# Kernel tuning notes

Measured on AMD Instinct MI355X. Metric: run time of the kernel, lower is better.

## Reference

```python
import jax, jax.numpy as jnp
import numpy as np


def setup_inputs() -> dict:
    key = jax.random.key(0)
    ks = jax.random.split(key, 7)
    B, C, H, W = 4, 64, 64, 64
    d = C // 8
    s = C ** -0.5  # 1x1-conv fan-in init scale
    x = jax.random.normal(ks[0], (B, C, H, W), jnp.float32)
    Wq = jax.random.normal(ks[1], (d, C), jnp.float32) * s
    bq = jnp.zeros((d,), jnp.float32)
    Wk = jax.random.normal(ks[2], (d, C), jnp.float32) * s
    bk = jnp.zeros((d,), jnp.float32)
    Wv = jax.random.normal(ks[3], (C, C), jnp.float32) * s
    bv = jnp.zeros((C,), jnp.float32)
    return {"x": x, "Wq": Wq, "bq": bq, "Wk": Wk, "bk": bk, "Wv": Wv, "bv": bv}


def reference(x, Wq, bq, Wk, bk, Wv, bv):
    B, C, H, W = x.shape
    N = H * W
    xf = x.reshape(B, C, N)                               # [B,C,N]
    # 1x1 convs == per-pixel channel matmuls
    q = jnp.einsum('dc,bcn->bnd', Wq, xf) + bq            # [B,N,d]
    k = jnp.einsum('dc,bcn->bnd', Wk, xf) + bk            # [B,N,d]
    v = jnp.einsum('ec,bcn->ben', Wv, xf) + bv[:, None]   # [B,C,N]
    # pairwise relative position offsets over flattened spatial grid
    idx = jnp.arange(N)
    col = (idx % W).astype(x.dtype)
    row = (idx // W).astype(x.dtype)
    col_diff = col[None, :] - col[:, None]                # [N,N], col_j - col_i
    row_diff = row[None, :] - row[:, None]                # [N,N]
    # scores = Q . (K + rel_pos folded into first two key channels)
    scores = jnp.einsum('bnd,bmd->bnm', q, k)             # [B,N,N]
    scores = scores + q[:, :, 0, None] * col_diff[None] + q[:, :, 1, None] * row_diff[None]
    attn = jax.nn.softmax(scores, axis=-1)                # softmax over keys
    out = jnp.einsum('bcm,bnm->bcn', v, attn)             # [B,C,N]
    return out.reshape(B, C, H, W)
```

## Files before the change

kernel.cpp:

```cpp
#include <hip/hip_runtime.h>

#define BB 4
#define CC 64
#define NN 4096

typedef __attribute__((ext_vector_type(8))) short short8;
typedef __attribute__((ext_vector_type(4))) float f32x4;
typedef __attribute__((ext_vector_type(4))) unsigned uint4v;

__device__ inline ushort f2bf(float x) {
    unsigned u = __float_as_uint(x);
    return (ushort)((u + 0x7fff + ((u >> 16) & 1)) >> 16);
}
__device__ inline float bf2f(ushort h) { return __uint_as_float(((unsigned)h) << 16); }

__device__ inline unsigned cvt_pk_bf16(float a, float b) {
    unsigned r;
    asm("v_cvt_pk_bf16_f32 %0, %1, %2" : "=v"(r) : "v"(a), "v"(b));
    return r;
}


__global__ __launch_bounds__(256) void qkv_kernel(
    const float* __restrict__ x,
    const float* __restrict__ Wq, const float* __restrict__ bq,
    const float* __restrict__ Wk, const float* __restrict__ bk,
    const float* __restrict__ Wv, const float* __restrict__ bv,
    ushort* __restrict__ qTp, ushort* __restrict__ kTp, ushort* __restrict__ vsw)
{
    const int blk = blockIdx.x;
    const int tid = threadIdx.x;

    if (blk < 64) {
        const int idx = blk * 256 + tid;
        const int b = idx >> 12, n = idx & (NN - 1);
        const float* xb = x + (size_t)b * CC * NN + n;
        float sq[8], sk[8];
#pragma unroll
        for (int d = 0; d < 8; ++d) { sq[d] = bq[d]; sk[d] = bk[d]; }
#pragma unroll 8
        for (int c = 0; c < CC; ++c) {
            const float xc = xb[c * NN];
#pragma unroll
            for (int d = 0; d < 8; ++d) {
                sq[d] += Wq[d * CC + c] * xc;
                sk[d] += Wk[d * CC + c] * xc;
            }
        }
        ushort hq[32], hk[32];
#pragma unroll
        for (int i = 0; i < 32; ++i) { hq[i] = 0; hk[i] = 0; }
#pragma unroll
        for (int d = 0; d < 8; ++d) { hq[d] = f2bf(sq[d]); hk[d] = f2bf(sk[d]); }
        hq[8]  = hq[0];
        hq[9]  = hq[1];
        hq[10] = f2bf(sq[0] - bf2f(hq[0]));
        hq[11] = f2bf(sq[1] - bf2f(hq[1]));
        const float col = (float)(n & 63), row = (float)(n >> 6);
        hk[8] = f2bf(col); hk[9] = f2bf(row); hk[10] = hk[8]; hk[11] = hk[9];

        uint4* dq = (uint4*)(qTp + (size_t)(b * NN + n) * 32);
        uint4* dk = (uint4*)(kTp + (size_t)(b * NN + n) * 32);
        const uint4* s4q = (const uint4*)hq;
        const uint4* s4k = (const uint4*)hk;
#pragma unroll
        for (int i = 0; i < 4; ++i) { dq[i] = s4q[i]; dk[i] = s4k[i]; }
        return;
    }

    const int w2 = blk - 64;
    const int pix = w2 >> 3, ec = w2 & 7;
    const int wvid = tid >> 6, lane = tid & 63;
    const int eu = __builtin_amdgcn_readfirstlane(ec * 4 + wvid);
    const int idx = pix * 64 + lane;
    const int b = idx >> 12, n = idx & (NN - 1);
    const float* xb = x + (size_t)b * CC * NN + n;
    float s0 = bv[eu], s1 = bv[eu + 32];
#pragma unroll 8
    for (int c = 0; c < CC; ++c) {
        const float xc = xb[c * NN];
        s0 += Wv[eu * CC + c] * xc;
        s1 += Wv[(eu + 32) * CC + c] * xc;
    }
    const int j = n & 63, t = n >> 6;
    const int kg = j >> 4, qd = (j >> 2) & 3, r = j & 3;
    const int sb = kg >> 1, jj = ((kg & 1) << 2) | r;
    const size_t tb = (size_t)(b * 64 + t) * 4096;
    const int e2 = eu + 32;
    vsw[tb + (size_t)(((sb * 4 + (eu >> 4)) * 64 + qd * 16 + (eu & 15)) * 8 + jj)] = f2bf(s0);
    vsw[tb + (size_t)(((sb * 4 + (e2 >> 4)) * 64 + qd * 16 + (e2 & 15)) * 8 + jj)] = f2bf(s1);
}

__global__ __launch_bounds__(512, 4) void attn_kernel(
    const ushort* __restrict__ qTp, const ushort* __restrict__ kTp,
    const ushort* __restrict__ vsw, float* __restrict__ out)
{
    const int blk = blockIdx.x;
    const int xcd = blk & 7, i8 = blk >> 3;
    const int b  = xcd >> 1;
    const int nq = (((xcd & 1) << 6) | i8) << 5;
    const int tid = threadIdx.x;
    const int wv = tid >> 6, lane = tid & 63;
    const int nn = lane & 15, quad = lane >> 4;

    __shared__ float Cb[8][1024];
    __shared__ float Mx[8][32];
    __shared__ float Db[8][32];
    __shared__ float dn[32];

    const short8 qf0 = *(const short8*)(qTp + ((size_t)(b * NN + nq + nn) * 32 + quad * 8));
    const short8 qf1 = *(const short8*)(qTp + ((size_t)(b * NN + nq + 16 + nn) * 32 + quad * 8));
    const ushort* kb = kTp + (size_t)b * NN * 32;

    float Ml0 = -1e30f, Ml1 = -1e30f;
    for (int t8 = 0; t8 < 8; ++t8) {
        const int t = wv * 8 + t8;
#pragma unroll
        for (int kg = 0; kg < 4; ++kg) {
            const short8 kf = *(const short8*)(kb + ((size_t)(t * 64 + kg * 16 + nn) * 32 + quad * 8));
            const f32x4 S0 = __builtin_amdgcn_mfma_f32_16x16x32_bf16(kf, qf0, (f32x4){0.f,0.f,0.f,0.f}, 0, 0, 0);
            const f32x4 S1 = __builtin_amdgcn_mfma_f32_16x16x32_bf16(kf, qf1, (f32x4){0.f,0.f,0.f,0.f}, 0, 0, 0);
            Ml0 = fmaxf(Ml0, fmaxf(fmaxf(S0[0], S0[1]), fmaxf(S0[2], S0[3])));
            Ml1 = fmaxf(Ml1, fmaxf(fmaxf(S1[0], S1[1]), fmaxf(S1[2], S1[3])));
        }
    }
    Ml0 = fmaxf(Ml0, __shfl_xor(Ml0, 16, 64));
    Ml0 = fmaxf(Ml0, __shfl_xor(Ml0, 32, 64));
    Ml1 = fmaxf(Ml1, __shfl_xor(Ml1, 16, 64));
    Ml1 = fmaxf(Ml1, __shfl_xor(Ml1, 32, 64));
    if (quad == 0) { Mx[wv][nn] = Ml0; Mx[wv][16 + nn] = Ml1; }
    __syncthreads();
    float M0 = Mx[0][nn], M1 = Mx[0][16 + nn];
#pragma unroll
    for (int w = 1; w < 8; ++w) { M0 = fmaxf(M0, Mx[w][nn]); M1 = fmaxf(M1, Mx[w][16 + nn]); }
    const f32x4 nM0 = {-M0, -M0, -M0, -M0};
    const f32x4 nM1 = {-M1, -M1, -M1, -M1};

    f32x4 acc0[4], acc1[4];
#pragma unroll
    for (int g = 0; g < 4; ++g) {
        acc0[g] = (f32x4){0.f,0.f,0.f,0.f};
        acc1[g] = (f32x4){0.f,0.f,0.f,0.f};
    }
    float dl0 = 0.f, dl1 = 0.f;

    for (int t8 = 0; t8 < 8; ++t8) {
        const int t = wv * 8 + t8;
        unsigned pw0[8], pw1[8];
#pragma unroll
        for (int kg = 0; kg < 4; ++kg) {
            const short8 kf = *(const short8*)(kb + ((size_t)(t * 64 + kg * 16 + nn) * 32 + quad * 8));
            const f32x4 S0 = __builtin_amdgcn_mfma_f32_16x16x32_bf16(kf, qf0, nM0, 0, 0, 0);
            const f32x4 S1 = __builtin_amdgcn_mfma_f32_16x16x32_bf16(kf, qf1, nM1, 0, 0, 0);
            const float w00 = __expf(S0[0]), w01 = __expf(S0[1]);
            const float w02 = __expf(S0[2]), w03 = __expf(S0[3]);
            const float w10 = __expf(S1[0]), w11 = __expf(S1[1]);
            const float w12 = __expf(S1[2]), w13 = __expf(S1[3]);
            dl0 += (w00 + w01) + (w02 + w03);
            dl1 += (w10 + w11) + (w12 + w13);
            pw0[2 * kg]     = cvt_pk_bf16(w00, w01);
            pw0[2 * kg + 1] = cvt_pk_bf16(w02, w03);
            pw1[2 * kg]     = cvt_pk_bf16(w10, w11);
            pw1[2 * kg + 1] = cvt_pk_bf16(w12, w13);
        }
        const uint4v u00 = {pw0[0], pw0[1], pw0[2], pw0[3]};
        const uint4v u01 = {pw0[4], pw0[5], pw0[6], pw0[7]};
        const uint4v u10 = {pw1[0], pw1[1], pw1[2], pw1[3]};
        const uint4v u11 = {pw1[4], pw1[5], pw1[6], pw1[7]};
        const short8 a00 = __builtin_bit_cast(short8, u00);
        const short8 a01 = __builtin_bit_cast(short8, u01);
        const short8 a10 = __builtin_bit_cast(short8, u10);
        const short8 a11 = __builtin_bit_cast(short8, u11);

        const ushort* vb = vsw + (size_t)(b * 64 + t) * 4096;
#pragma unroll
        for (int g = 0; g < 4; ++g) {
            const short8 vf = *(const short8*)(vb + g * 512 + lane * 8);
            acc0[g] = __builtin_amdgcn_mfma_f32_16x16x32_bf16(a00, vf, acc0[g], 0, 0, 0);
            acc1[g] = __builtin_amdgcn_mfma_f32_16x16x32_bf16(a10, vf, acc1[g], 0, 0, 0);
        }
#pragma unroll
        for (int g = 0; g < 4; ++g) {
            const short8 vf = *(const short8*)(vb + 2048 + g * 512 + lane * 8);
            acc0[g] = __builtin_amdgcn_mfma_f32_16x16x32_bf16(a01, vf, acc0[g], 0, 0, 0);
            acc1[g] = __builtin_amdgcn_mfma_f32_16x16x32_bf16(a11, vf, acc1[g], 0, 0, 0);
        }
    }

    dl0 += __shfl_xor(dl0, 16, 64); dl0 += __shfl_xor(dl0, 32, 64);
    dl1 += __shfl_xor(dl1, 16, 64); dl1 += __shfl_xor(dl1, 32, 64);
    if (quad == 0) { Db[wv][nn] = dl0; Db[wv][16 + nn] = dl1; }

#pragma unroll
    for (int g = 0; g < 4; ++g)
#pragma unroll
        for (int r = 0; r < 4; ++r)
            Cb[wv][(g * 4 + r) * 64 + lane] = acc0[g][r];
    __syncthreads();

    if (tid < 32) {
        float s = Db[0][tid];
#pragma unroll
        for (int w = 1; w < 8; ++w) s += Db[w][tid];
        dn[tid] = s;
    }
    __syncthreads();

#pragma unroll
    for (int it = 0; it < 2; ++it) {
        const int e = tid + it * 512;
        const int q = e & 15, c = e >> 4;
        const int src = ((c >> 4) * 4 + (q & 3)) * 64 + (q >> 2) * 16 + (c & 15);
        float v = Cb[0][src];
#pragma unroll
        for (int w = 1; w < 8; ++w) v += Cb[w][src];
        out[(size_t)(b * CC + c) * NN + nq + q] = v / dn[q];
    }
    __syncthreads();

#pragma unroll
    for (int g = 0; g < 4; ++g)
#pragma unroll
        for (int r = 0; r < 4; ++r)
            Cb[wv][(g * 4 + r) * 64 + lane] = acc1[g][r];
    __syncthreads();

#pragma unroll
    for (int it = 0; it < 2; ++it) {
        const int e = tid + it * 512;
        const int q = e & 15, c = e >> 4;
        const int src = ((c >> 4) * 4 + (q & 3)) * 64 + (q >> 2) * 16 + (c & 15);
        float v = Cb[0][src];
#pragma unroll
        for (int w = 1; w < 8; ++w) v += Cb[w][src];
        out[(size_t)(b * CC + c) * NN + nq + 16 + q] = v / dn[16 + q];
    }
}

extern "C" void kernel_launch(void* const* d_in, const int* in_sizes, int n_in,
                              void* d_out, int out_size, void* d_ws, size_t ws_size,
                              hipStream_t stream) {
    const float* x  = (const float*)d_in[0];
    const float* Wq = (const float*)d_in[1];
    const float* bq = (const float*)d_in[2];
    const float* Wk = (const float*)d_in[3];
    const float* bk = (const float*)d_in[4];
    const float* Wv = (const float*)d_in[5];
    const float* bv = (const float*)d_in[6];
    float* out = (float*)d_out;

    ushort* ws  = (ushort*)d_ws;
    ushort* qTp = ws;
    ushort* kTp = ws + (size_t)BB * NN * 32;
    ushort* vsw = ws + (size_t)2 * BB * NN * 32;

    qkv_kernel<<<2112, 256, 0, stream>>>(x, Wq, bq, Wk, bk, Wv, bv, qTp, kTp, vsw);
    attn_kernel<<<512, 512, 0, stream>>>(qTp, kTp, vsw, out);
}
```

Before: 114.3 us.

## Replace two-pass softmax max with online lazy-rescaled softmax; widen V projection per thread

The attention kernel no longer runs a full first pass over all keys to find the row max. It seeds the running max from the first tile and then rescales the accumulators and denominator only when a tile's max exceeds the current one. A final cross-wave merge rescales each wave's partials to the global max. This removes about half of the QK^T MFMA work and K loads, at the cost of per-tile max reductions, shuffles and occasional rescale branches. Separately, the V projection now computes four output channels per thread instead of two, halving the number of V blocks launched.

```diff
diff --git a/kernel.cpp b/kernel.cpp
--- a/kernel.cpp
+++ b/kernel.cpp
@@ -69,26 +69,31 @@
     }
 
     const int w2 = blk - 64;
-    const int pix = w2 >> 3, ec = w2 & 7;
-    const int wvid = tid >> 6, lane = tid & 63;
-    const int eu = __builtin_amdgcn_readfirstlane(ec * 4 + wvid);
+    const int pix = w2 >> 2, ec = w2 & 3;
+    const int lane = tid & 63;
+    const int eu = __builtin_amdgcn_readfirstlane(ec * 4 + (tid >> 6));
     const int idx = pix * 64 + lane;
     const int b = idx >> 12, n = idx & (NN - 1);
     const float* xb = x + (size_t)b * CC * NN + n;
-    float s0 = bv[eu], s1 = bv[eu + 32];
+    float s0 = bv[eu], s1 = bv[eu + 16], s2 = bv[eu + 32], s3 = bv[eu + 48];
 #pragma unroll 8
     for (int c = 0; c < CC; ++c) {
         const float xc = xb[c * NN];
         s0 += Wv[eu * CC + c] * xc;
-        s1 += Wv[(eu + 32) * CC + c] * xc;
+        s1 += Wv[(eu + 16) * CC + c] * xc;
+        s2 += Wv[(eu + 32) * CC + c] * xc;
+        s3 += Wv[(eu + 48) * CC + c] * xc;
     }
     const int j = n & 63, t = n >> 6;
     const int kg = j >> 4, qd = (j >> 2) & 3, r = j & 3;
     const int sb = kg >> 1, jj = ((kg & 1) << 2) | r;
     const size_t tb = (size_t)(b * 64 + t) * 4096;
-    const int e2 = eu + 32;
-    vsw[tb + (size_t)(((sb * 4 + (eu >> 4)) * 64 + qd * 16 + (eu & 15)) * 8 + jj)] = f2bf(s0);
-    vsw[tb + (size_t)(((sb * 4 + (e2 >> 4)) * 64 + qd * 16 + (e2 & 15)) * 8 + jj)] = f2bf(s1);
+    const float sv[4] = {s0, s1, s2, s3};
+#pragma unroll
+    for (int u = 0; u < 4; ++u) {
+        const int e = eu + u * 16;
+        vsw[tb + (size_t)(((sb * 4 + (e >> 4)) * 64 + qd * 16 + (e & 15)) * 8 + jj)] = f2bf(sv[u]);
+    }
 }
 
 __global__ __launch_bounds__(512, 4) void attn_kernel(
@@ -112,29 +117,24 @@
     const short8 qf1 = *(const short8*)(qTp + ((size_t)(b * NN + nq + 16 + nn) * 32 + quad * 8));
     const ushort* kb = kTp + (size_t)b * NN * 32;
 
-    float Ml0 = -1e30f, Ml1 = -1e30f;
-    for (int t8 = 0; t8 < 8; ++t8) {
-        const int t = wv * 8 + t8;
+    float m0 = -1e30f, m1 = -1e30f;
+    {
+        const int t = wv * 8;
 #pragma unroll
         for (int kg = 0; kg < 4; ++kg) {
             const short8 kf = *(const short8*)(kb + ((size_t)(t * 64 + kg * 16 + nn) * 32 + quad * 8));
             const f32x4 S0 = __builtin_amdgcn_mfma_f32_16x16x32_bf16(kf, qf0, (f32x4){0.f,0.f,0.f,0.f}, 0, 0, 0);
             const f32x4 S1 = __builtin_amdgcn_mfma_f32_16x16x32_bf16(kf, qf1, (f32x4){0.f,0.f,0.f,0.f}, 0, 0, 0);
-            Ml0 = fmaxf(Ml0, fmaxf(fmaxf(S0[0], S0[1]), fmaxf(S0[2], S0[3])));
-            Ml1 = fmaxf(Ml1, fmaxf(fmaxf(S1[0], S1[1]), fmaxf(S1[2], S1[3])));
-        }
-    }
-    Ml0 = fmaxf(Ml0, __shfl_xor(Ml0, 16, 64));
-    Ml0 = fmaxf(Ml0, __shfl_xor(Ml0, 32, 64));
-    Ml1 = fmaxf(Ml1, __shfl_xor(Ml1, 16, 64));
-    Ml1 = fmaxf(Ml1, __shfl_xor(Ml1, 32, 64));
-    if (quad == 0) { Mx[wv][nn] = Ml0; Mx[wv][16 + nn] = Ml1; }
-    __syncthreads();
-    float M0 = Mx[0][nn], M1 = Mx[0][16 + nn];
-#pragma unroll
-    for (int w = 1; w < 8; ++w) { M0 = fmaxf(M0, Mx[w][nn]); M1 = fmaxf(M1, Mx[w][16 + nn]); }
-    const f32x4 nM0 = {-M0, -M0, -M0, -M0};
-    const f32x4 nM1 = {-M1, -M1, -M1, -M1};
+            m0 = fmaxf(m0, fmaxf(fmaxf(S0[0], S0[1]), fmaxf(S0[2], S0[3])));
+            m1 = fmaxf(m1, fmaxf(fmaxf(S1[0], S1[1]), fmaxf(S1[2], S1[3])));
+        }
+        m0 = fmaxf(m0, __shfl_xor(m0, 16, 64));
+        m0 = fmaxf(m0, __shfl_xor(m0, 32, 64));
+        m1 = fmaxf(m1, __shfl_xor(m1, 16, 64));
+        m1 = fmaxf(m1, __shfl_xor(m1, 32, 64));
+    }
+    f32x4 nM0 = {-m0, -m0, -m0, -m0};
+    f32x4 nM1 = {-m1, -m1, -m1, -m1};
 
     f32x4 acc0[4], acc1[4];
 #pragma unroll
@@ -146,16 +146,52 @@
 
     for (int t8 = 0; t8 < 8; ++t8) {
         const int t = wv * 8 + t8;
-        unsigned pw0[8], pw1[8];
+        f32x4 s0[4], s1[4];
 #pragma unroll
         for (int kg = 0; kg < 4; ++kg) {
             const short8 kf = *(const short8*)(kb + ((size_t)(t * 64 + kg * 16 + nn) * 32 + quad * 8));
-            const f32x4 S0 = __builtin_amdgcn_mfma_f32_16x16x32_bf16(kf, qf0, nM0, 0, 0, 0);
-            const f32x4 S1 = __builtin_amdgcn_mfma_f32_16x16x32_bf16(kf, qf1, nM1, 0, 0, 0);
-            const float w00 = __expf(S0[0]), w01 = __expf(S0[1]);
-            const float w02 = __expf(S0[2]), w03 = __expf(S0[3]);
-            const float w10 = __expf(S1[0]), w11 = __expf(S1[1]);
-            const float w12 = __expf(S1[2]), w13 = __expf(S1[3]);
+            s0[kg] = __builtin_amdgcn_mfma_f32_16x16x32_bf16(kf, qf0, nM0, 0, 0, 0);
+            s1[kg] = __builtin_amdgcn_mfma_f32_16x16x32_bf16(kf, qf1, nM1, 0, 0, 0);
+        }
+        float r0 = fmaxf(fmaxf(s0[0][0], s0[0][1]), fmaxf(s0[0][2], s0[0][3]));
+        float r1 = fmaxf(fmaxf(s1[0][0], s1[0][1]), fmaxf(s1[0][2], s1[0][3]));
+#pragma unroll
+        for (int kg = 1; kg < 4; ++kg) {
+            r0 = fmaxf(r0, fmaxf(fmaxf(s0[kg][0], s0[kg][1]), fmaxf(s0[kg][2], s0[kg][3])));
+            r1 = fmaxf(r1, fmaxf(fmaxf(s1[kg][0], s1[kg][1]), fmaxf(s1[kg][2], s1[kg][3])));
+        }
+        r0 = fmaxf(r0, __shfl_xor(r0, 16, 64));
+        r0 = fmaxf(r0, __shfl_xor(r0, 32, 64));
+        r1 = fmaxf(r1, __shfl_xor(r1, 16, 64));
+        r1 = fmaxf(r1, __shfl_xor(r1, 32, 64));
+
+        if (__any((r0 > 0.f) || (r1 > 0.f))) {
+            const float d0 = fmaxf(r0, 0.f), d1 = fmaxf(r1, 0.f);
+            const float e0 = __expf(-d0), e1 = __expf(-d1);
+            m0 += d0; m1 += d1;
+            nM0 = (f32x4){-m0, -m0, -m0, -m0};
+            nM1 = (f32x4){-m1, -m1, -m1, -m1};
+            dl0 *= e0; dl1 *= e1;
+            f32x4 e0v, e1v;
+#pragma unroll
+            for (int rr = 0; rr < 4; ++rr) {
+                e0v[rr] = __shfl(e0, quad * 4 + rr, 64);
+                e1v[rr] = __shfl(e1, quad * 4 + rr, 64);
+            }
+#pragma unroll
+            for (int g = 0; g < 4; ++g) { acc0[g] *= e0v; acc1[g] *= e1v; }
+            const f32x4 dv0 = {d0, d0, d0, d0}, dv1 = {d1, d1, d1, d1};
+#pragma unroll
+            for (int kg = 0; kg < 4; ++kg) { s0[kg] -= dv0; s1[kg] -= dv1; }
+        }
+
+        unsigned pw0[8], pw1[8];
+#pragma unroll
+        for (int kg = 0; kg < 4; ++kg) {
+            const float w00 = __expf(s0[kg][0]), w01 = __expf(s0[kg][1]);
+            const float w02 = __expf(s0[kg][2]), w03 = __expf(s0[kg][3]);
+            const float w10 = __expf(s1[kg][0]), w11 = __expf(s1[kg][1]);
+            const float w12 = __expf(s1[kg][2]), w13 = __expf(s1[kg][3]);
             dl0 += (w00 + w01) + (w02 + w03);
             dl1 += (w10 + w11) + (w12 + w13);
             pw0[2 * kg]     = cvt_pk_bf16(w00, w01);
@@ -186,6 +222,22 @@
             acc1[g] = __builtin_amdgcn_mfma_f32_16x16x32_bf16(a11, vf, acc1[g], 0, 0, 0);
         }
     }
+
+    if (quad == 0) { Mx[wv][nn] = m0; Mx[wv][16 + nn] = m1; }
+    __syncthreads();
+    float M0 = Mx[0][nn], M1 = Mx[0][16 + nn];
+#pragma unroll
+    for (int w = 1; w < 8; ++w) { M0 = fmaxf(M0, Mx[w][nn]); M1 = fmaxf(M1, Mx[w][16 + nn]); }
+    const float g0 = __expf(m0 - M0), g1 = __expf(m1 - M1);
+    dl0 *= g0; dl1 *= g1;
+    f32x4 g0v, g1v;
+#pragma unroll
+    for (int rr = 0; rr < 4; ++rr) {
+        g0v[rr] = __shfl(g0, quad * 4 + rr, 64);
+        g1v[rr] = __shfl(g1, quad * 4 + rr, 64);
+    }
+#pragma unroll
+    for (int g = 0; g < 4; ++g) { acc0[g] *= g0v; acc1[g] *= g1v; }
 
     dl0 += __shfl_xor(dl0, 16, 64); dl0 += __shfl_xor(dl0, 32, 64);
     dl1 += __shfl_xor(dl1, 16, 64); dl1 += __shfl_xor(dl1, 32, 64);
@@ -254,6 +306,6 @@
     ushort* kTp = ws + (size_t)BB * NN * 32;
     ushort* vsw = ws + (size_t)2 * BB * NN * 32;
 
-    qkv_kernel<<<2112, 256, 0, stream>>>(x, Wq, bq, Wk, bk, Wv, bv, qTp, kTp, vsw);
+    qkv_kernel<<<1088, 256, 0, stream>>>(x, Wq, bq, Wk, bk, Wv, bv, qTp, kTp, vsw);
     attn_kernel<<<512, 512, 0, stream>>>(qTp, kTp, vsw, out);
 }
```

After: 115.6 us. About the same (+1.1%).
